# Optimization experiments

Hardware: AMD Instinct MI355X
Metric: run time of the kernel (lower is better)

## Reference

```python
import jax, jax.numpy as jnp
import numpy as np

N = 50000      # nodes
E = 800000     # edges (avg degree 16)
IN, H, OUT = 128, 128, 64


def setup_inputs() -> dict:
    key = jax.random.key(0)
    k1, k2, k3, k4 = jax.random.split(key, 4)
    x = jax.random.normal(k1, (N, IN), dtype=jnp.float32)
    edge_index = jax.random.randint(k2, (2, E), 0, N, dtype=jnp.int32)
    W1 = jax.random.normal(k3, (IN, H), dtype=jnp.float32) * (1.0 / np.sqrt(IN))
    b1 = jnp.zeros((H,), dtype=jnp.float32)
    W2 = jax.random.normal(k4, (H, OUT), dtype=jnp.float32) * (1.0 / np.sqrt(H))
    b2 = jnp.zeros((OUT,), dtype=jnp.float32)
    return {"x": x, "edge_index": edge_index, "W1": W1, "b1": b1, "W2": W2, "b2": b2}


def gcn_conv(x, edge_index, W, b):
    """PyG GCNConv: D^-1/2 (A + I) D^-1/2 (x W) + b, with self-loops."""
    src, dst = edge_index[0], edge_index[1]
    h = x @ W                                              # [N, F_out] transform first (F_out <= F_in path)
    ones = jnp.ones((src.shape[0],), dtype=h.dtype)
    deg = jax.ops.segment_sum(ones, dst, num_segments=N) + 1.0  # +1 for self-loop
    inv_sqrt_deg = jax.lax.rsqrt(deg)
    norm = inv_sqrt_deg[src] * inv_sqrt_deg[dst]           # [E]
    agg = jax.ops.segment_sum(h[src] * norm[:, None], dst, num_segments=N)
    # self-loop contribution: norm_ii = deg_i^-1
    return agg + h * (1.0 / deg)[:, None] + b


def reference(x, edge_index, W1, b1, W2, b2):
    h = jax.nn.relu(gcn_conv(x, edge_index, W1, b1))
    return gcn_conv(h, edge_index, W2, b2)
```

## Files before the change

kernel.cpp:

```cpp
#include <hip/hip_runtime.h>
#include <hip/hip_bf16.h>


#define GCN_IN   128
#define GCN_H    128
#define GCN_OUT  64
#define CAP      64
#define OVF_CAP  65536
#define SCAT_BLOCKS 2048

using short8 = __attribute__((ext_vector_type(8))) short;
using f32x4  = __attribute__((ext_vector_type(4))) float;

__device__ __forceinline__ ushort f2bf(float f) {
    uint b = __float_as_uint(f);
    b = (b + 0x7FFFu + ((b >> 16) & 1u)) >> 16;
    return (ushort)b;
}
__device__ __forceinline__ float bf2f_lo(uint u) { return __uint_as_float(u << 16); }
__device__ __forceinline__ float bf2f_hi(uint u) { return __uint_as_float(u & 0xFFFF0000u); }

__global__ __launch_bounds__(256) void k_scatter(
        const int* __restrict__ src, const int* __restrict__ dst,
        int* __restrict__ cnt, ushort* __restrict__ slot,
        int* __restrict__ ovfcnt, int2* __restrict__ ovf, int E, int N) {
    const int part = blockIdx.x & 7;
    const int psz  = (N + 7) >> 3;
    const int lo   = part * psz;
    const int hi   = min(lo + psz, N);
    const int bip  = blockIdx.x >> 3;
    const int stride = (SCAT_BLOCKS >> 3) * 256;
    for (int e = bip * 256 + threadIdx.x; e < E; e += stride) {
        int d = __builtin_nontemporal_load(dst + e);
        int s = __builtin_nontemporal_load(src + e);
        if (d >= lo && d < hi) {
            int pos = atomicAdd(&cnt[d], 1);
            if (pos < CAP) {
                slot[(size_t)d * CAP + pos] = (ushort)s;
            } else {
                int q = atomicAdd(ovfcnt, 1);
                if (q < OVF_CAP) ovf[q] = make_int2(d, s);
            }
        }
    }
}

__global__ __launch_bounds__(256) void k_gemm1(const float* __restrict__ A,
                                               const float* __restrict__ B,
                                               const int* __restrict__ cnt,
                                               ushort* __restrict__ C, int M) {
    __shared__ __align__(16) ushort As[64][136];
    __shared__ __align__(16) ushort Bs[128][136];
    const int tid  = threadIdx.x;
    const int w    = tid >> 6;
    const int lane = tid & 63;
    const int l15  = lane & 15;
    const int q8   = (lane >> 4) * 8;
    const int row0 = blockIdx.x * 64;

    #pragma unroll
    for (int t = 0; t < 8; ++t) {
        int f = tid * 4 + t * 1024;
        int r = f >> 7;
        int k = f & 127;
        float4 v = make_float4(0.f, 0.f, 0.f, 0.f);
        int gr = row0 + r;
        if (gr < M) v = *(const float4*)(A + (size_t)gr * 128 + k);
        ushort4 o;
        o.x = f2bf(v.x); o.y = f2bf(v.y); o.z = f2bf(v.z); o.w = f2bf(v.w);
        *(ushort4*)&As[r][k] = o;
    }
    #pragma unroll
    for (int t = 0; t < 16; ++t) {
        int f = tid * 4 + t * 1024;
        int k = f >> 7;
        int n = f & 127;
        float4 v = *(const float4*)(B + (size_t)k * 128 + n);
        Bs[n + 0][k] = f2bf(v.x);
        Bs[n + 1][k] = f2bf(v.y);
        Bs[n + 2][k] = f2bf(v.z);
        Bs[n + 3][k] = f2bf(v.w);
    }
    __syncthreads();

    f32x4 acc[8];
    #pragma unroll
    for (int t = 0; t < 8; ++t) {
        acc[t][0] = 0.f; acc[t][1] = 0.f; acc[t][2] = 0.f; acc[t][3] = 0.f;
    }
    #pragma unroll
    for (int kt = 0; kt < 4; ++kt) {
        short8 a = *(const short8*)&As[16 * w + l15][32 * kt + q8];
        #pragma unroll
        for (int t = 0; t < 8; ++t) {
            short8 b = *(const short8*)&Bs[16 * t + l15][32 * kt + q8];
            acc[t] = __builtin_amdgcn_mfma_f32_16x16x32_bf16(a, b, acc[t], 0, 0, 0);
        }
    }
    const int quad = lane >> 4;
    #pragma unroll
    for (int r = 0; r < 4; ++r) {
        int grow = row0 + 16 * w + quad * 4 + r;
        if (grow < M) {
            float ws = rsqrtf((float)(cnt[grow] + 1));
            #pragma unroll
            for (int t = 0; t < 8; ++t) {
                C[(size_t)grow * 128 + 16 * t + l15] = f2bf(ws * acc[t][r]);
            }
        }
    }
}

__global__ __launch_bounds__(256) void k_gemm2(const ushort* __restrict__ A,
                                               const float* __restrict__ B,
                                               const int* __restrict__ cnt,
                                               ushort* __restrict__ C, int M) {
    __shared__ __align__(16) ushort As[64][136];
    __shared__ __align__(16) ushort Bs[64][136];
    const int tid  = threadIdx.x;
    const int w    = tid >> 6;
    const int lane = tid & 63;
    const int l15  = lane & 15;
    const int q8   = (lane >> 4) * 8;
    const int row0 = blockIdx.x * 64;

    #pragma unroll
    for (int t = 0; t < 4; ++t) {
        int f = tid * 8 + t * 2048;
        int r = f >> 7;
        int k = f & 127;
        uint4 v = make_uint4(0u, 0u, 0u, 0u);
        int gr = row0 + r;
        if (gr < M) v = *(const uint4*)(A + (size_t)gr * 128 + k);
        *(uint4*)&As[r][k] = v;
    }
    #pragma unroll
    for (int t = 0; t < 8; ++t) {
        int f = tid * 4 + t * 1024;
        int k = f >> 6;
        int n = f & 63;
        float4 v = *(const float4*)(B + (size_t)k * 64 + n);
        Bs[n + 0][k] = f2bf(v.x);
        Bs[n + 1][k] = f2bf(v.y);
        Bs[n + 2][k] = f2bf(v.z);
        Bs[n + 3][k] = f2bf(v.w);
    }
    __syncthreads();

    f32x4 acc[4];
    #pragma unroll
    for (int t = 0; t < 4; ++t) {
        acc[t][0] = 0.f; acc[t][1] = 0.f; acc[t][2] = 0.f; acc[t][3] = 0.f;
    }
    #pragma unroll
    for (int kt = 0; kt < 4; ++kt) {
        short8 a = *(const short8*)&As[16 * w + l15][32 * kt + q8];
        #pragma unroll
        for (int t = 0; t < 4; ++t) {
            short8 b = *(const short8*)&Bs[16 * t + l15][32 * kt + q8];
            acc[t] = __builtin_amdgcn_mfma_f32_16x16x32_bf16(a, b, acc[t], 0, 0, 0);
        }
    }
    const int quad = lane >> 4;
    #pragma unroll
    for (int r = 0; r < 4; ++r) {
        int grow = row0 + 16 * w + quad * 4 + r;
        if (grow < M) {
            float ws = rsqrtf((float)(cnt[grow] + 1));
            #pragma unroll
            for (int t = 0; t < 4; ++t) {
                C[(size_t)grow * 64 + 16 * t + l15] = f2bf(ws * acc[t][r]);
            }
        }
    }
}

__global__ __launch_bounds__(256) void k_agg128(const ushort* __restrict__ h,
                                                const int* __restrict__ cnt,
                                                const ushort* __restrict__ slot,
                                                const float* __restrict__ bias,
                                                const int* __restrict__ ovfcnt,
                                                const int2* __restrict__ ovf,
                                                ushort* __restrict__ out, int n) {
    int node = (blockIdx.x * 256 + threadIdx.x) >> 6;
    int lane = threadIdx.x & 63;
    if (node >= n) return;
    int deg = cnt[node];
    int degm = min(deg, CAP);
    float isd_i = rsqrtf((float)(deg + 1));
    int sidx = (int)__builtin_nontemporal_load(slot + (size_t)node * CAP + lane);

    const int q = lane >> 4;
    const int i = lane & 15;
    const ushort* hp = h + 8 * i;

    float acc[8] = {};
    for (int j = 0; j < degm; j += 8) {
        int j0 = j + q;
        int j1 = j + 4 + q;
        int   s0 = __shfl(sidx, j0);
        int   s1 = __shfl(sidx, j1);
        float w0 = (j0 < degm) ? 1.f : 0.f;
        float w1 = (j1 < degm) ? 1.f : 0.f;
        uint4 v0 = *(const uint4*)(hp + (size_t)s0 * 128);
        uint4 v1 = *(const uint4*)(hp + (size_t)s1 * 128);
        acc[0] += w0 * bf2f_lo(v0.x) + w1 * bf2f_lo(v1.x);
        acc[1] += w0 * bf2f_hi(v0.x) + w1 * bf2f_hi(v1.x);
        acc[2] += w0 * bf2f_lo(v0.y) + w1 * bf2f_lo(v1.y);
        acc[3] += w0 * bf2f_hi(v0.y) + w1 * bf2f_hi(v1.y);
        acc[4] += w0 * bf2f_lo(v0.z) + w1 * bf2f_lo(v1.z);
        acc[5] += w0 * bf2f_hi(v0.z) + w1 * bf2f_hi(v1.z);
        acc[6] += w0 * bf2f_lo(v0.w) + w1 * bf2f_lo(v1.w);
        acc[7] += w0 * bf2f_hi(v0.w) + w1 * bf2f_hi(v1.w);
    }
    int ovn = *ovfcnt;
    for (int t = 0; t < ovn; ++t) {
        int2 p = ovf[t];
        if (p.x == node && q == 0) {
            uint4 v0 = *(const uint4*)(hp + (size_t)p.y * 128);
            acc[0] += bf2f_lo(v0.x); acc[1] += bf2f_hi(v0.x);
            acc[2] += bf2f_lo(v0.y); acc[3] += bf2f_hi(v0.y);
            acc[4] += bf2f_lo(v0.z); acc[5] += bf2f_hi(v0.z);
            acc[6] += bf2f_lo(v0.w); acc[7] += bf2f_hi(v0.w);
        }
    }
    #pragma unroll
    for (int k = 0; k < 8; ++k) {
        acc[k] += __shfl_xor(acc[k], 16);
        acc[k] += __shfl_xor(acc[k], 32);
    }
    if (q == 0) {
        uint4 vs = *(const uint4*)(hp + (size_t)node * 128);
        float4 ba = *(const float4*)(bias + 8 * i);
        float4 bb = *(const float4*)(bias + 8 * i + 4);
        float r0 = fmaxf((acc[0] + bf2f_lo(vs.x)) * isd_i + ba.x, 0.f);
        float r1 = fmaxf((acc[1] + bf2f_hi(vs.x)) * isd_i + ba.y, 0.f);
        float r2 = fmaxf((acc[2] + bf2f_lo(vs.y)) * isd_i + ba.z, 0.f);
        float r3 = fmaxf((acc[3] + bf2f_hi(vs.y)) * isd_i + ba.w, 0.f);
        float r4 = fmaxf((acc[4] + bf2f_lo(vs.z)) * isd_i + bb.x, 0.f);
        float r5 = fmaxf((acc[5] + bf2f_hi(vs.z)) * isd_i + bb.y, 0.f);
        float r6 = fmaxf((acc[6] + bf2f_lo(vs.w)) * isd_i + bb.z, 0.f);
        float r7 = fmaxf((acc[7] + bf2f_hi(vs.w)) * isd_i + bb.w, 0.f);
        uint4 o;
        o.x = (uint)f2bf(r0) | ((uint)f2bf(r1) << 16);
        o.y = (uint)f2bf(r2) | ((uint)f2bf(r3) << 16);
        o.z = (uint)f2bf(r4) | ((uint)f2bf(r5) << 16);
        o.w = (uint)f2bf(r6) | ((uint)f2bf(r7) << 16);
        *(uint4*)(out + (size_t)node * 128 + 8 * i) = o;
    }
}

__global__ __launch_bounds__(256) void k_agg64(const ushort* __restrict__ h,
                                               const int* __restrict__ cnt,
                                               const ushort* __restrict__ slot,
                                               const float* __restrict__ bias,
                                               const int* __restrict__ ovfcnt,
                                               const int2* __restrict__ ovf,
                                               float* __restrict__ out, int n) {
    int node = (blockIdx.x * 256 + threadIdx.x) >> 6;
    int lane = threadIdx.x & 63;
    if (node >= n) return;
    int deg = cnt[node];
    int degm = min(deg, CAP);
    float isd_i = rsqrtf((float)(deg + 1));
    int sidx = (int)__builtin_nontemporal_load(slot + (size_t)node * CAP + lane);

    const int g = lane >> 3;
    const int i = lane & 7;
    const ushort* hp = h + 8 * i;

    float acc[8] = {};
    for (int j = 0; j < degm; j += 16) {
        int j0 = j + g;
        int j1 = j + 8 + g;
        int   s0 = __shfl(sidx, j0);
        int   s1 = __shfl(sidx, j1);
        float w0 = (j0 < degm) ? 1.f : 0.f;
        float w1 = (j1 < degm) ? 1.f : 0.f;
        uint4 v0 = *(const uint4*)(hp + (size_t)s0 * 64);
        uint4 v1 = *(const uint4*)(hp + (size_t)s1 * 64);
        acc[0] += w0 * bf2f_lo(v0.x) + w1 * bf2f_lo(v1.x);
        acc[1] += w0 * bf2f_hi(v0.x) + w1 * bf2f_hi(v1.x);
        acc[2] += w0 * bf2f_lo(v0.y) + w1 * bf2f_lo(v1.y);
        acc[3] += w0 * bf2f_hi(v0.y) + w1 * bf2f_hi(v1.y);
        acc[4] += w0 * bf2f_lo(v0.z) + w1 * bf2f_lo(v1.z);
        acc[5] += w0 * bf2f_hi(v0.z) + w1 * bf2f_hi(v1.z);
        acc[6] += w0 * bf2f_lo(v0.w) + w1 * bf2f_lo(v1.w);
        acc[7] += w0 * bf2f_hi(v0.w) + w1 * bf2f_hi(v1.w);
    }
    int ovn = *ovfcnt;
    for (int t = 0; t < ovn; ++t) {
        int2 p = ovf[t];
        if (p.x == node && g == 0) {
            uint4 v0 = *(const uint4*)(hp + (size_t)p.y * 64);
            acc[0] += bf2f_lo(v0.x); acc[1] += bf2f_hi(v0.x);
            acc[2] += bf2f_lo(v0.y); acc[3] += bf2f_hi(v0.y);
            acc[4] += bf2f_lo(v0.z); acc[5] += bf2f_hi(v0.z);
            acc[6] += bf2f_lo(v0.w); acc[7] += bf2f_hi(v0.w);
        }
    }
    #pragma unroll
    for (int k = 0; k < 8; ++k) {
        acc[k] += __shfl_xor(acc[k], 8);
        acc[k] += __shfl_xor(acc[k], 16);
        acc[k] += __shfl_xor(acc[k], 32);
    }
    if (g == 0) {
        uint4 vs = *(const uint4*)(hp + (size_t)node * 64);
        float4 ba = *(const float4*)(bias + 8 * i);
        float4 bb = *(const float4*)(bias + 8 * i + 4);
        float4 r0, r1;
        r0.x = (acc[0] + bf2f_lo(vs.x)) * isd_i + ba.x;
        r0.y = (acc[1] + bf2f_hi(vs.x)) * isd_i + ba.y;
        r0.z = (acc[2] + bf2f_lo(vs.y)) * isd_i + ba.z;
        r0.w = (acc[3] + bf2f_hi(vs.y)) * isd_i + ba.w;
        r1.x = (acc[4] + bf2f_lo(vs.z)) * isd_i + bb.x;
        r1.y = (acc[5] + bf2f_hi(vs.z)) * isd_i + bb.y;
        r1.z = (acc[6] + bf2f_lo(vs.w)) * isd_i + bb.z;
        r1.w = (acc[7] + bf2f_hi(vs.w)) * isd_i + bb.w;
        float* op = out + (size_t)node * 64 + 8 * i;
        *(float4*)op = r0;
        *(float4*)(op + 4) = r1;
    }
}

static inline size_t align256(size_t x) { return (x + 255) & ~(size_t)255; }

extern "C" void kernel_launch(void* const* d_in, const int* in_sizes, int n_in,
                              void* d_out, int out_size, void* d_ws, size_t ws_size,
                              hipStream_t stream) {
    const float* x  = (const float*)d_in[0];
    const int*   ei = (const int*)d_in[1];
    const float* W1 = (const float*)d_in[2];
    const float* b1 = (const float*)d_in[3];
    const float* W2 = (const float*)d_in[4];
    const float* b2 = (const float*)d_in[5];
    float* out = (float*)d_out;

    const int N = in_sizes[0] / GCN_IN;
    const int E = in_sizes[1] / 2;
    const int* src = ei;
    const int* dst = ei + E;

    char* ws = (char*)d_ws;
    size_t o = 0;
    int*    cnt    = (int*)(ws + o);     o += align256((size_t)N * 4);
    int*    ovfcnt = (int*)(ws + o);     o += 256;
    int2*   ovf    = (int2*)(ws + o);    o += align256((size_t)OVF_CAP * 8);
    ushort* slot   = (ushort*)(ws + o);  o += align256((size_t)N * CAP * 2);
    ushort* hb     = (ushort*)(ws + o);  o += align256((size_t)N * GCN_H * 2);
    ushort* h1b    = (ushort*)(ws + o);  o += align256((size_t)N * GCN_H * 2);
    ushort* h2b    = (ushort*)(ws + o);  o += align256((size_t)N * GCN_OUT * 2);

    hipMemsetAsync(cnt, 0, align256((size_t)N * 4) + 256, stream);

    k_scatter<<<SCAT_BLOCKS, 256, 0, stream>>>(src, dst, cnt, slot,
                                               ovfcnt, ovf, E, N);

    k_gemm1<<<(N + 63) / 64, 256, 0, stream>>>(x, W1, cnt, hb, N);

    k_agg128<<<(N * 64 + 255) / 256, 256, 0, stream>>>(hb, cnt, slot, b1,
                                                       ovfcnt, ovf, h1b, N);
    k_gemm2<<<(N + 63) / 64, 256, 0, stream>>>(h1b, W2, cnt, h2b, N);

    k_agg64<<<(N * 64 + 255) / 256, 256, 0, stream>>>(h2b, cnt, slot, b2,
                                                      ovfcnt, ovf, out, N);
}
```

Measured before the change: 205.6 us.

## Bucket neighbor slots by source range and compact overflow into slots

The scatter now reads four edges at a time with vector loads and splits each node's 64 slots into 8 buckets of 8, chosen by source-id range. The goal is rough source ordering inside each adjacency row and less contention on a single per-node counter. A new compaction kernel packs the buckets with ballot/popcount, merges overflow edges into the slot row, and writes the final degree and clamped degree. Both aggregation kernels drop their per-node linear scan of the overflow list. The cost is an extra kernel launch and an 8x larger counter array to clear and read. The vector loads also assume E is a multiple of 4.

```diff
diff --git a/kernel.cpp b/kernel.cpp
--- a/kernel.cpp
+++ b/kernel.cpp
@@ -5,12 +5,12 @@
 #define GCN_IN   128
 #define GCN_H    128
 #define GCN_OUT  64
-#define CAP      64
 #define OVF_CAP  65536
 #define SCAT_BLOCKS 2048
 
 using short8 = __attribute__((ext_vector_type(8))) short;
 using f32x4  = __attribute__((ext_vector_type(4))) float;
+using int4v  = __attribute__((ext_vector_type(4))) int;
 
 __device__ __forceinline__ ushort f2bf(float f) {
     uint b = __float_as_uint(f);
@@ -22,26 +22,71 @@
 
 __global__ __launch_bounds__(256) void k_scatter(
         const int* __restrict__ src, const int* __restrict__ dst,
-        int* __restrict__ cnt, ushort* __restrict__ slot,
-        int* __restrict__ ovfcnt, int2* __restrict__ ovf, int E, int N) {
+        int* __restrict__ cnt8, ushort* __restrict__ slot,
+        int* __restrict__ ovfcnt, int2* __restrict__ ovf,
+        int E, int N, float pscale) {
     const int part = blockIdx.x & 7;
     const int psz  = (N + 7) >> 3;
     const int lo   = part * psz;
     const int hi   = min(lo + psz, N);
     const int bip  = blockIdx.x >> 3;
-    const int stride = (SCAT_BLOCKS >> 3) * 256;
-    for (int e = bip * 256 + threadIdx.x; e < E; e += stride) {
-        int d = __builtin_nontemporal_load(dst + e);
-        int s = __builtin_nontemporal_load(src + e);
-        if (d >= lo && d < hi) {
-            int pos = atomicAdd(&cnt[d], 1);
-            if (pos < CAP) {
-                slot[(size_t)d * CAP + pos] = (ushort)s;
-            } else {
-                int q = atomicAdd(ovfcnt, 1);
-                if (q < OVF_CAP) ovf[q] = make_int2(d, s);
+    const int stride4 = (SCAT_BLOCKS >> 3) * 256 * 4;
+    for (int e = (bip * 256 + threadIdx.x) * 4; e < E; e += stride4) {
+        int4v d4 = __builtin_nontemporal_load((const int4v*)(dst + e));
+        int4v s4 = __builtin_nontemporal_load((const int4v*)(src + e));
+        #pragma unroll
+        for (int k = 0; k < 4; ++k) {
+            int d = d4[k];
+            int s = s4[k];
+            if (d >= lo && d < hi) {
+                int p = min((int)((float)s * pscale), 7);
+                int pos = atomicAdd(&cnt8[d * 8 + p], 1);
+                if (pos < 8) {
+                    slot[(size_t)d * 64 + p * 8 + pos] = (ushort)s;
+                } else {
+                    int q = atomicAdd(ovfcnt, 1);
+                    if (q < OVF_CAP) ovf[q] = make_int2(d, s);
+                }
             }
         }
+    }
+}
+
+__global__ __launch_bounds__(256) void k_compact(
+        ushort* __restrict__ slot, const int* __restrict__ cnt8,
+        int* __restrict__ cnt, int* __restrict__ degs,
+        const int* __restrict__ ovfcnt, const int2* __restrict__ ovf, int N) {
+    int node = (blockIdx.x * 256 + threadIdx.x) >> 6;
+    int lane = threadIdx.x & 63;
+    if (node >= N) return;
+    int np = cnt8[node * 8 + (lane >> 3)];
+    bool valid = (lane & 7) < np;
+    ushort v = slot[(size_t)node * 64 + lane];
+    unsigned long long mask = __ballot(valid);
+    int total = __popcll(mask);
+    int pos = __popcll(mask & ((1ull << lane) - 1ull));
+    if (valid) slot[(size_t)node * 64 + pos] = v;
+    int appended = 0;
+    int ovn = *ovfcnt;
+    for (int q = 0; q < ovn; q += 64) {
+        int ex = -1, ey = 0;
+        if (q + lane < ovn) {
+            int2 e = ovf[q + lane];
+            ex = e.x; ey = e.y;
+        }
+        bool m = (ex == node);
+        unsigned long long mb = __ballot(m);
+        if (m) {
+            int ai = __popcll(mb & ((1ull << lane) - 1ull));
+            int wp = total + appended + ai;
+            if (wp < 64) slot[(size_t)node * 64 + wp] = (ushort)ey;
+        }
+        appended += __popcll(mb);
+    }
+    if (lane == 0) {
+        int deg = total + appended;
+        cnt[node]  = deg;
+        degs[node] = min(deg, 64);
     }
 }
 
@@ -177,18 +222,16 @@
 
 __global__ __launch_bounds__(256) void k_agg128(const ushort* __restrict__ h,
                                                 const int* __restrict__ cnt,
+                                                const int* __restrict__ degs,
                                                 const ushort* __restrict__ slot,
                                                 const float* __restrict__ bias,
-                                                const int* __restrict__ ovfcnt,
-                                                const int2* __restrict__ ovf,
                                                 ushort* __restrict__ out, int n) {
     int node = (blockIdx.x * 256 + threadIdx.x) >> 6;
     int lane = threadIdx.x & 63;
     if (node >= n) return;
-    int deg = cnt[node];
-    int degm = min(deg, CAP);
-    float isd_i = rsqrtf((float)(deg + 1));
-    int sidx = (int)__builtin_nontemporal_load(slot + (size_t)node * CAP + lane);
+    int degm = degs[node];
+    float isd_i = rsqrtf((float)(cnt[node] + 1));
+    int sidx = (int)__builtin_nontemporal_load(slot + (size_t)node * 64 + lane);
 
     const int q = lane >> 4;
     const int i = lane & 15;
@@ -213,17 +256,6 @@
         acc[6] += w0 * bf2f_lo(v0.w) + w1 * bf2f_lo(v1.w);
         acc[7] += w0 * bf2f_hi(v0.w) + w1 * bf2f_hi(v1.w);
     }
-    int ovn = *ovfcnt;
-    for (int t = 0; t < ovn; ++t) {
-        int2 p = ovf[t];
-        if (p.x == node && q == 0) {
-            uint4 v0 = *(const uint4*)(hp + (size_t)p.y * 128);
-            acc[0] += bf2f_lo(v0.x); acc[1] += bf2f_hi(v0.x);
-            acc[2] += bf2f_lo(v0.y); acc[3] += bf2f_hi(v0.y);
-            acc[4] += bf2f_lo(v0.z); acc[5] += bf2f_hi(v0.z);
-            acc[6] += bf2f_lo(v0.w); acc[7] += bf2f_hi(v0.w);
-        }
-    }
     #pragma unroll
     for (int k = 0; k < 8; ++k) {
         acc[k] += __shfl_xor(acc[k], 16);
@@ -252,18 +284,16 @@
 
 __global__ __launch_bounds__(256) void k_agg64(const ushort* __restrict__ h,
                                                const int* __restrict__ cnt,
+                                               const int* __restrict__ degs,
                                                const ushort* __restrict__ slot,
                                                const float* __restrict__ bias,
-                                               const int* __restrict__ ovfcnt,
-                                               const int2* __restrict__ ovf,
                                                float* __restrict__ out, int n) {
     int node = (blockIdx.x * 256 + threadIdx.x) >> 6;
     int lane = threadIdx.x & 63;
     if (node >= n) return;
-    int deg = cnt[node];
-    int degm = min(deg, CAP);
-    float isd_i = rsqrtf((float)(deg + 1));
-    int sidx = (int)__builtin_nontemporal_load(slot + (size_t)node * CAP + lane);
+    int degm = degs[node];
+    float isd_i = rsqrtf((float)(cnt[node] + 1));
+    int sidx = (int)__builtin_nontemporal_load(slot + (size_t)node * 64 + lane);
 
     const int g = lane >> 3;
     const int i = lane & 7;
@@ -288,17 +318,6 @@
         acc[6] += w0 * bf2f_lo(v0.w) + w1 * bf2f_lo(v1.w);
         acc[7] += w0 * bf2f_hi(v0.w) + w1 * bf2f_hi(v1.w);
     }
-    int ovn = *ovfcnt;
-    for (int t = 0; t < ovn; ++t) {
-        int2 p = ovf[t];
-        if (p.x == node && g == 0) {
-            uint4 v0 = *(const uint4*)(hp + (size_t)p.y * 64);
-            acc[0] += bf2f_lo(v0.x); acc[1] += bf2f_hi(v0.x);
-            acc[2] += bf2f_lo(v0.y); acc[3] += bf2f_hi(v0.y);
-            acc[4] += bf2f_lo(v0.z); acc[5] += bf2f_hi(v0.z);
-            acc[6] += bf2f_lo(v0.w); acc[7] += bf2f_hi(v0.w);
-        }
-    }
     #pragma unroll
     for (int k = 0; k < 8; ++k) {
         acc[k] += __shfl_xor(acc[k], 8);
@@ -344,25 +363,30 @@
 
     char* ws = (char*)d_ws;
     size_t o = 0;
-    int*    cnt    = (int*)(ws + o);     o += align256((size_t)N * 4);
+    int*    cnt8   = (int*)(ws + o);     o += align256((size_t)N * 8 * 4);
     int*    ovfcnt = (int*)(ws + o);     o += 256;
     int2*   ovf    = (int2*)(ws + o);    o += align256((size_t)OVF_CAP * 8);
-    ushort* slot   = (ushort*)(ws + o);  o += align256((size_t)N * CAP * 2);
+    ushort* slot   = (ushort*)(ws + o);  o += align256((size_t)N * 64 * 2);
+    int*    cnt    = (int*)(ws + o);     o += align256((size_t)N * 4);
+    int*    degs   = (int*)(ws + o);     o += align256((size_t)N * 4);
     ushort* hb     = (ushort*)(ws + o);  o += align256((size_t)N * GCN_H * 2);
     ushort* h1b    = (ushort*)(ws + o);  o += align256((size_t)N * GCN_H * 2);
     ushort* h2b    = (ushort*)(ws + o);  o += align256((size_t)N * GCN_OUT * 2);
 
-    hipMemsetAsync(cnt, 0, align256((size_t)N * 4) + 256, stream);
-
-    k_scatter<<<SCAT_BLOCKS, 256, 0, stream>>>(src, dst, cnt, slot,
-                                               ovfcnt, ovf, E, N);
+    (void)hipMemsetAsync(cnt8, 0, align256((size_t)N * 8 * 4) + 256, stream);
+
+    k_scatter<<<SCAT_BLOCKS, 256, 0, stream>>>(src, dst, cnt8, slot,
+                                               ovfcnt, ovf, E, N, 8.0f / (float)N);
+
+    k_compact<<<(N * 64 + 255) / 256, 256, 0, stream>>>(slot, cnt8, cnt, degs,
+                                                        ovfcnt, ovf, N);
 
     k_gemm1<<<(N + 63) / 64, 256, 0, stream>>>(x, W1, cnt, hb, N);
 
-    k_agg128<<<(N * 64 + 255) / 256, 256, 0, stream>>>(hb, cnt, slot, b1,
-                                                       ovfcnt, ovf, h1b, N);
+    k_agg128<<<(N * 64 + 255) / 256, 256, 0, stream>>>(hb, cnt, degs, slot, b1,
+                                                       h1b, N);
     k_gemm2<<<(N + 63) / 64, 256, 0, stream>>>(h1b, W2, cnt, h2b, N);
 
-    k_agg64<<<(N * 64 + 255) / 256, 256, 0, stream>>>(h2b, cnt, slot, b2,
-                                                      ovfcnt, ovf, out, N);
-}
+    k_agg64<<<(N * 64 + 255) / 256, 256, 0, stream>>>(h2b, cnt, degs, slot, b2,
+                                                      out, N);
+}
```

Result: slower. 216.2 us (+5.1%).

## Fuse scatter with GEMM1 and fold GEMM2 into layer-1 aggregation

Applied to the files above, without the earlier changes.

Merges the edge scatter and the first GEMM into one launch so they run side by side. Because the GEMM no longer waits for degrees, source-side normalization moves into the aggregation as per-neighbor weights gathered from cnt. The second GEMM is folded into the layer-1 aggregation kernel: each wave's aggregated row goes to LDS and is multiplied by W2 with scalar FMAs. This drops one launch and the h1 round trip through memory, at the cost of extra per-edge cnt gathers, a W2 reload into LDS per 4-node block, and scalar dot products in place of MFMA.

```diff
diff --git a/kernel.cpp b/kernel.cpp
--- a/kernel.cpp
+++ b/kernel.cpp
@@ -11,6 +11,7 @@
 
 using short8 = __attribute__((ext_vector_type(8))) short;
 using f32x4  = __attribute__((ext_vector_type(4))) float;
+using int4v  = __attribute__((ext_vector_type(4))) int;
 
 __device__ __forceinline__ ushort f2bf(float f) {
     uint b = __float_as_uint(f);
@@ -20,233 +21,217 @@
 __device__ __forceinline__ float bf2f_lo(uint u) { return __uint_as_float(u << 16); }
 __device__ __forceinline__ float bf2f_hi(uint u) { return __uint_as_float(u & 0xFFFF0000u); }
 
-__global__ __launch_bounds__(256) void k_scatter(
+__global__ __launch_bounds__(256) void k_fused1(
         const int* __restrict__ src, const int* __restrict__ dst,
         int* __restrict__ cnt, ushort* __restrict__ slot,
-        int* __restrict__ ovfcnt, int2* __restrict__ ovf, int E, int N) {
-    const int part = blockIdx.x & 7;
-    const int psz  = (N + 7) >> 3;
-    const int lo   = part * psz;
-    const int hi   = min(lo + psz, N);
-    const int bip  = blockIdx.x >> 3;
-    const int stride = (SCAT_BLOCKS >> 3) * 256;
-    for (int e = bip * 256 + threadIdx.x; e < E; e += stride) {
-        int d = __builtin_nontemporal_load(dst + e);
-        int s = __builtin_nontemporal_load(src + e);
-        if (d >= lo && d < hi) {
-            int pos = atomicAdd(&cnt[d], 1);
-            if (pos < CAP) {
-                slot[(size_t)d * CAP + pos] = (ushort)s;
-            } else {
-                int q = atomicAdd(ovfcnt, 1);
-                if (q < OVF_CAP) ovf[q] = make_int2(d, s);
+        int* __restrict__ ovfcnt, int2* __restrict__ ovf, int E,
+        const float* __restrict__ A, const float* __restrict__ B,
+        ushort* __restrict__ C, int M, int N) {
+    __shared__ __align__(16) ushort As[64][40];
+    __shared__ __align__(16) ushort Bs[128][40];
+    const int tid = threadIdx.x;
+
+    if (blockIdx.x < SCAT_BLOCKS) {
+        const int part = blockIdx.x & 7;
+        const int psz  = (N + 7) >> 3;
+        const int lo   = part * psz;
+        const int hi   = min(lo + psz, N);
+        const int bip  = blockIdx.x >> 3;
+        const int stride4 = (SCAT_BLOCKS >> 3) * 256 * 4;
+        for (int e = (bip * 256 + tid) * 4; e < E; e += stride4) {
+            int4v d4 = __builtin_nontemporal_load((const int4v*)(dst + e));
+            int4v s4 = __builtin_nontemporal_load((const int4v*)(src + e));
+            #pragma unroll
+            for (int k = 0; k < 4; ++k) {
+                int d = d4[k];
+                int s = s4[k];
+                if (d >= lo && d < hi) {
+                    int pos = atomicAdd(&cnt[d], 1);
+                    if (pos < CAP) {
+                        slot[(size_t)d * CAP + pos] = (ushort)s;
+                    } else {
+                        int q = atomicAdd(ovfcnt, 1);
+                        if (q < OVF_CAP) ovf[q] = make_int2(d, s);
+                    }
+                }
             }
         }
-    }
-}
-
-__global__ __launch_bounds__(256) void k_gemm1(const float* __restrict__ A,
-                                               const float* __restrict__ B,
-                                               const int* __restrict__ cnt,
-                                               ushort* __restrict__ C, int M) {
-    __shared__ __align__(16) ushort As[64][136];
-    __shared__ __align__(16) ushort Bs[128][136];
-    const int tid  = threadIdx.x;
+        return;
+    }
+
+    const int g    = blockIdx.x - SCAT_BLOCKS;
+    const int row0 = g * 64;
     const int w    = tid >> 6;
     const int lane = tid & 63;
     const int l15  = lane & 15;
     const int q8   = (lane >> 4) * 8;
-    const int row0 = blockIdx.x * 64;
-
-    #pragma unroll
-    for (int t = 0; t < 8; ++t) {
-        int f = tid * 4 + t * 1024;
-        int r = f >> 7;
-        int k = f & 127;
-        float4 v = make_float4(0.f, 0.f, 0.f, 0.f);
-        int gr = row0 + r;
-        if (gr < M) v = *(const float4*)(A + (size_t)gr * 128 + k);
-        ushort4 o;
-        o.x = f2bf(v.x); o.y = f2bf(v.y); o.z = f2bf(v.z); o.w = f2bf(v.w);
-        *(ushort4*)&As[r][k] = o;
-    }
-    #pragma unroll
-    for (int t = 0; t < 16; ++t) {
-        int f = tid * 4 + t * 1024;
-        int k = f >> 7;
-        int n = f & 127;
-        float4 v = *(const float4*)(B + (size_t)k * 128 + n);
-        Bs[n + 0][k] = f2bf(v.x);
-        Bs[n + 1][k] = f2bf(v.y);
-        Bs[n + 2][k] = f2bf(v.z);
-        Bs[n + 3][k] = f2bf(v.w);
-    }
-    __syncthreads();
 
     f32x4 acc[8];
     #pragma unroll
     for (int t = 0; t < 8; ++t) {
         acc[t][0] = 0.f; acc[t][1] = 0.f; acc[t][2] = 0.f; acc[t][3] = 0.f;
     }
-    #pragma unroll
-    for (int kt = 0; kt < 4; ++kt) {
-        short8 a = *(const short8*)&As[16 * w + l15][32 * kt + q8];
+    for (int kb = 0; kb < 128; kb += 32) {
+        #pragma unroll
+        for (int tt = 0; tt < 2; ++tt) {
+            int f = tid * 4 + tt * 1024;
+            int r = f >> 5;
+            int k = f & 31;
+            float4 v = make_float4(0.f, 0.f, 0.f, 0.f);
+            int gr = row0 + r;
+            if (gr < M) v = *(const float4*)(A + (size_t)gr * 128 + kb + k);
+            ushort4 o;
+            o.x = f2bf(v.x); o.y = f2bf(v.y); o.z = f2bf(v.z); o.w = f2bf(v.w);
+            *(ushort4*)&As[r][k] = o;
+        }
+        #pragma unroll
+        for (int tt = 0; tt < 4; ++tt) {
+            int f = tid * 4 + tt * 1024;
+            int k = f >> 7;
+            int n = f & 127;
+            float4 v = *(const float4*)(B + (size_t)(kb + k) * 128 + n);
+            Bs[n + 0][k] = f2bf(v.x);
+            Bs[n + 1][k] = f2bf(v.y);
+            Bs[n + 2][k] = f2bf(v.z);
+            Bs[n + 3][k] = f2bf(v.w);
+        }
+        __syncthreads();
+        short8 a = *(const short8*)&As[16 * w + l15][q8];
         #pragma unroll
         for (int t = 0; t < 8; ++t) {
-            short8 b = *(const short8*)&Bs[16 * t + l15][32 * kt + q8];
+            short8 b = *(const short8*)&Bs[16 * t + l15][q8];
             acc[t] = __builtin_amdgcn_mfma_f32_16x16x32_bf16(a, b, acc[t], 0, 0, 0);
         }
+        __syncthreads();
     }
     const int quad = lane >> 4;
     #pragma unroll
     for (int r = 0; r < 4; ++r) {
         int grow = row0 + 16 * w + quad * 4 + r;
         if (grow < M) {
-            float ws = rsqrtf((float)(cnt[grow] + 1));
             #pragma unroll
             for (int t = 0; t < 8; ++t) {
-                C[(size_t)grow * 128 + 16 * t + l15] = f2bf(ws * acc[t][r]);
+                __builtin_nontemporal_store(
+                    f2bf(acc[t][r]), C + (size_t)grow * 128 + 16 * t + l15);
             }
         }
     }
 }
 
-__global__ __launch_bounds__(256) void k_gemm2(const ushort* __restrict__ A,
-                                               const float* __restrict__ B,
-                                               const int* __restrict__ cnt,
-                                               ushort* __restrict__ C, int M) {
-    __shared__ __align__(16) ushort As[64][136];
-    __shared__ __align__(16) ushort Bs[64][136];
+__global__ __launch_bounds__(256) void k_agg128g2(
+        const ushort* __restrict__ h,
+        const int* __restrict__ cnt,
+        const ushort* __restrict__ slot,
+        const float* __restrict__ bias,
+        const int* __restrict__ ovfcnt,
+        const int2* __restrict__ ovf,
+        const float* __restrict__ W2,
+        ushort* __restrict__ h2b,
+        int n) {
+    __shared__ __align__(16) ushort W2s[64][136];
+    __shared__ __align__(16) ushort h1s[4][136];
     const int tid  = threadIdx.x;
     const int w    = tid >> 6;
     const int lane = tid & 63;
-    const int l15  = lane & 15;
-    const int q8   = (lane >> 4) * 8;
-    const int row0 = blockIdx.x * 64;
+    const int node = blockIdx.x * 4 + w;
 
     #pragma unroll
-    for (int t = 0; t < 4; ++t) {
-        int f = tid * 8 + t * 2048;
-        int r = f >> 7;
-        int k = f & 127;
-        uint4 v = make_uint4(0u, 0u, 0u, 0u);
-        int gr = row0 + r;
-        if (gr < M) v = *(const uint4*)(A + (size_t)gr * 128 + k);
-        *(uint4*)&As[r][k] = v;
-    }
-    #pragma unroll
-    for (int t = 0; t < 8; ++t) {
-        int f = tid * 4 + t * 1024;
+    for (int tt = 0; tt < 8; ++tt) {
+        int f = tid * 4 + tt * 1024;
         int k = f >> 6;
-        int n = f & 63;
-        float4 v = *(const float4*)(B + (size_t)k * 64 + n);
-        Bs[n + 0][k] = f2bf(v.x);
-        Bs[n + 1][k] = f2bf(v.y);
-        Bs[n + 2][k] = f2bf(v.z);
-        Bs[n + 3][k] = f2bf(v.w);
+        int nn = f & 63;
+        float4 v = *(const float4*)(W2 + (size_t)k * 64 + nn);
+        W2s[nn + 0][k] = f2bf(v.x);
+        W2s[nn + 1][k] = f2bf(v.y);
+        W2s[nn + 2][k] = f2bf(v.z);
+        W2s[nn + 3][k] = f2bf(v.w);
+    }
+
+    float isd_i = 0.f;
+    if (node < n) {
+        int deg = cnt[node];
+        int degm = min(deg, CAP);
+        isd_i = rsqrtf((float)(deg + 1));
+        int sidx = (int)__builtin_nontemporal_load(slot + (size_t)node * CAP + lane);
+        bool valid = lane < degm;
+        if (!valid) sidx = 0;
+        float wl = valid ? rsqrtf((float)(cnt[sidx] + 1)) : 0.f;
+
+        const int q = lane >> 4;
+        const int i = lane & 15;
+        const ushort* hp = h + 8 * i;
+
+        float acc[8] = {};
+        for (int j = 0; j < degm; j += 8) {
+            int j0 = j + q;
+            int j1 = j + 4 + q;
+            int   s0 = __shfl(sidx, j0);
+            int   s1 = __shfl(sidx, j1);
+            float w0 = __shfl(wl, j0);
+            float w1 = __shfl(wl, j1);
+            uint4 v0 = *(const uint4*)(hp + (size_t)s0 * 128);
+            uint4 v1 = *(const uint4*)(hp + (size_t)s1 * 128);
+            acc[0] += w0 * bf2f_lo(v0.x) + w1 * bf2f_lo(v1.x);
+            acc[1] += w0 * bf2f_hi(v0.x) + w1 * bf2f_hi(v1.x);
+            acc[2] += w0 * bf2f_lo(v0.y) + w1 * bf2f_lo(v1.y);
+            acc[3] += w0 * bf2f_hi(v0.y) + w1 * bf2f_hi(v1.y);
+            acc[4] += w0 * bf2f_lo(v0.z) + w1 * bf2f_lo(v1.z);
+            acc[5] += w0 * bf2f_hi(v0.z) + w1 * bf2f_hi(v1.z);
+            acc[6] += w0 * bf2f_lo(v0.w) + w1 * bf2f_lo(v1.w);
+            acc[7] += w0 * bf2f_hi(v0.w) + w1 * bf2f_hi(v1.w);
+        }
+        int ovn = *ovfcnt;
+        for (int t = 0; t < ovn; ++t) {
+            int2 p = ovf[t];
+            if (p.x == node && q == 0) {
+                float w0 = rsqrtf((float)(cnt[p.y] + 1));
+                uint4 v0 = *(const uint4*)(hp + (size_t)p.y * 128);
+                acc[0] += w0 * bf2f_lo(v0.x); acc[1] += w0 * bf2f_hi(v0.x);
+                acc[2] += w0 * bf2f_lo(v0.y); acc[3] += w0 * bf2f_hi(v0.y);
+                acc[4] += w0 * bf2f_lo(v0.z); acc[5] += w0 * bf2f_hi(v0.z);
+                acc[6] += w0 * bf2f_lo(v0.w); acc[7] += w0 * bf2f_hi(v0.w);
+            }
+        }
+        #pragma unroll
+        for (int k = 0; k < 8; ++k) {
+            acc[k] += __shfl_xor(acc[k], 16);
+            acc[k] += __shfl_xor(acc[k], 32);
+        }
+        if (q == 0) {
+            uint4 vs = *(const uint4*)(hp + (size_t)node * 128);
+            float4 ba = *(const float4*)(bias + 8 * i);
+            float4 bb = *(const float4*)(bias + 8 * i + 4);
+            float r0 = fmaxf((acc[0] + isd_i * bf2f_lo(vs.x)) * isd_i + ba.x, 0.f);
+            float r1 = fmaxf((acc[1] + isd_i * bf2f_hi(vs.x)) * isd_i + ba.y, 0.f);
+            float r2 = fmaxf((acc[2] + isd_i * bf2f_lo(vs.y)) * isd_i + ba.z, 0.f);
+            float r3 = fmaxf((acc[3] + isd_i * bf2f_hi(vs.y)) * isd_i + ba.w, 0.f);
+            float r4 = fmaxf((acc[4] + isd_i * bf2f_lo(vs.z)) * isd_i + bb.x, 0.f);
+            float r5 = fmaxf((acc[5] + isd_i * bf2f_hi(vs.z)) * isd_i + bb.y, 0.f);
+            float r6 = fmaxf((acc[6] + isd_i * bf2f_lo(vs.w)) * isd_i + bb.z, 0.f);
+            float r7 = fmaxf((acc[7] + isd_i * bf2f_hi(vs.w)) * isd_i + bb.w, 0.f);
+            uint4 o;
+            o.x = (uint)f2bf(r0) | ((uint)f2bf(r1) << 16);
+            o.y = (uint)f2bf(r2) | ((uint)f2bf(r3) << 16);
+            o.z = (uint)f2bf(r4) | ((uint)f2bf(r5) << 16);
+            o.w = (uint)f2bf(r6) | ((uint)f2bf(r7) << 16);
+            *(uint4*)&h1s[w][8 * i] = o;
+        }
     }
     __syncthreads();
 
-    f32x4 acc[4];
-    #pragma unroll
-    for (int t = 0; t < 4; ++t) {
-        acc[t][0] = 0.f; acc[t][1] = 0.f; acc[t][2] = 0.f; acc[t][3] = 0.f;
-    }
-    #pragma unroll
-    for (int kt = 0; kt < 4; ++kt) {
-        short8 a = *(const short8*)&As[16 * w + l15][32 * kt + q8];
-        #pragma unroll
-        for (int t = 0; t < 4; ++t) {
-            short8 b = *(const short8*)&Bs[16 * t + l15][32 * kt + q8];
-            acc[t] = __builtin_amdgcn_mfma_f32_16x16x32_bf16(a, b, acc[t], 0, 0, 0);
-        }
-    }
-    const int quad = lane >> 4;
-    #pragma unroll
-    for (int r = 0; r < 4; ++r) {
-        int grow = row0 + 16 * w + quad * 4 + r;
-        if (grow < M) {
-            float ws = rsqrtf((float)(cnt[grow] + 1));
-            #pragma unroll
-            for (int t = 0; t < 4; ++t) {
-                C[(size_t)grow * 64 + 16 * t + l15] = f2bf(ws * acc[t][r]);
-            }
-        }
-    }
-}
-
-__global__ __launch_bounds__(256) void k_agg128(const ushort* __restrict__ h,
-                                                const int* __restrict__ cnt,
-                                                const ushort* __restrict__ slot,
-                                                const float* __restrict__ bias,
-                                                const int* __restrict__ ovfcnt,
-                                                const int2* __restrict__ ovf,
-                                                ushort* __restrict__ out, int n) {
-    int node = (blockIdx.x * 256 + threadIdx.x) >> 6;
-    int lane = threadIdx.x & 63;
-    if (node >= n) return;
-    int deg = cnt[node];
-    int degm = min(deg, CAP);
-    float isd_i = rsqrtf((float)(deg + 1));
-    int sidx = (int)__builtin_nontemporal_load(slot + (size_t)node * CAP + lane);
-
-    const int q = lane >> 4;
-    const int i = lane & 15;
-    const ushort* hp = h + 8 * i;
-
-    float acc[8] = {};
-    for (int j = 0; j < degm; j += 8) {
-        int j0 = j + q;
-        int j1 = j + 4 + q;
-        int   s0 = __shfl(sidx, j0);
-        int   s1 = __shfl(sidx, j1);
-        float w0 = (j0 < degm) ? 1.f : 0.f;
-        float w1 = (j1 < degm) ? 1.f : 0.f;
-        uint4 v0 = *(const uint4*)(hp + (size_t)s0 * 128);
-        uint4 v1 = *(const uint4*)(hp + (size_t)s1 * 128);
-        acc[0] += w0 * bf2f_lo(v0.x) + w1 * bf2f_lo(v1.x);
-        acc[1] += w0 * bf2f_hi(v0.x) + w1 * bf2f_hi(v1.x);
-        acc[2] += w0 * bf2f_lo(v0.y) + w1 * bf2f_lo(v1.y);
-        acc[3] += w0 * bf2f_hi(v0.y) + w1 * bf2f_hi(v1.y);
-        acc[4] += w0 * bf2f_lo(v0.z) + w1 * bf2f_lo(v1.z);
-        acc[5] += w0 * bf2f_hi(v0.z) + w1 * bf2f_hi(v1.z);
-        acc[6] += w0 * bf2f_lo(v0.w) + w1 * bf2f_lo(v1.w);
-        acc[7] += w0 * bf2f_hi(v0.w) + w1 * bf2f_hi(v1.w);
-    }
-    int ovn = *ovfcnt;
-    for (int t = 0; t < ovn; ++t) {
-        int2 p = ovf[t];
-        if (p.x == node && q == 0) {
-            uint4 v0 = *(const uint4*)(hp + (size_t)p.y * 128);
-            acc[0] += bf2f_lo(v0.x); acc[1] += bf2f_hi(v0.x);
-            acc[2] += bf2f_lo(v0.y); acc[3] += bf2f_hi(v0.y);
-            acc[4] += bf2f_lo(v0.z); acc[5] += bf2f_hi(v0.z);
-            acc[6] += bf2f_lo(v0.w); acc[7] += bf2f_hi(v0.w);
-        }
-    }
-    #pragma unroll
-    for (int k = 0; k < 8; ++k) {
-        acc[k] += __shfl_xor(acc[k], 16);
-        acc[k] += __shfl_xor(acc[k], 32);
-    }
-    if (q == 0) {
-        uint4 vs = *(const uint4*)(hp + (size_t)node * 128);
-        float4 ba = *(const float4*)(bias + 8 * i);
-        float4 bb = *(const float4*)(bias + 8 * i + 4);
-        float r0 = fmaxf((acc[0] + bf2f_lo(vs.x)) * isd_i + ba.x, 0.f);
-        float r1 = fmaxf((acc[1] + bf2f_hi(vs.x)) * isd_i + ba.y, 0.f);
-        float r2 = fmaxf((acc[2] + bf2f_lo(vs.y)) * isd_i + ba.z, 0.f);
-        float r3 = fmaxf((acc[3] + bf2f_hi(vs.y)) * isd_i + ba.w, 0.f);
-        float r4 = fmaxf((acc[4] + bf2f_lo(vs.z)) * isd_i + bb.x, 0.f);
-        float r5 = fmaxf((acc[5] + bf2f_hi(vs.z)) * isd_i + bb.y, 0.f);
-        float r6 = fmaxf((acc[6] + bf2f_lo(vs.w)) * isd_i + bb.z, 0.f);
-        float r7 = fmaxf((acc[7] + bf2f_hi(vs.w)) * isd_i + bb.w, 0.f);
-        uint4 o;
-        o.x = (uint)f2bf(r0) | ((uint)f2bf(r1) << 16);
-        o.y = (uint)f2bf(r2) | ((uint)f2bf(r3) << 16);
-        o.z = (uint)f2bf(r4) | ((uint)f2bf(r5) << 16);
-        o.w = (uint)f2bf(r6) | ((uint)f2bf(r7) << 16);
-        *(uint4*)(out + (size_t)node * 128 + 8 * i) = o;
+    if (node < n) {
+        float s = 0.f;
+        #pragma unroll
+        for (int kk = 0; kk < 16; ++kk) {
+            uint4 hv = *(const uint4*)&h1s[w][8 * kk];
+            uint4 wv = *(const uint4*)&W2s[lane][8 * kk];
+            s += bf2f_lo(hv.x) * bf2f_lo(wv.x) + bf2f_hi(hv.x) * bf2f_hi(wv.x);
+            s += bf2f_lo(hv.y) * bf2f_lo(wv.y) + bf2f_hi(hv.y) * bf2f_hi(wv.y);
+            s += bf2f_lo(hv.z) * bf2f_lo(wv.z) + bf2f_hi(hv.z) * bf2f_hi(wv.z);
+            s += bf2f_lo(hv.w) * bf2f_lo(wv.w) + bf2f_hi(hv.w) * bf2f_hi(wv.w);
+        }
+        __builtin_nontemporal_store(f2bf(isd_i * s),
+                                    h2b + (size_t)node * 64 + lane);
     }
 }
 
@@ -349,19 +334,18 @@
     int2*   ovf    = (int2*)(ws + o);    o += align256((size_t)OVF_CAP * 8);
     ushort* slot   = (ushort*)(ws + o);  o += align256((size_t)N * CAP * 2);
     ushort* hb     = (ushort*)(ws + o);  o += align256((size_t)N * GCN_H * 2);
-    ushort* h1b    = (ushort*)(ws + o);  o += align256((size_t)N * GCN_H * 2);
     ushort* h2b    = (ushort*)(ws + o);  o += align256((size_t)N * GCN_OUT * 2);
 
-    hipMemsetAsync(cnt, 0, align256((size_t)N * 4) + 256, stream);
-
-    k_scatter<<<SCAT_BLOCKS, 256, 0, stream>>>(src, dst, cnt, slot,
-                                               ovfcnt, ovf, E, N);
-
-    k_gemm1<<<(N + 63) / 64, 256, 0, stream>>>(x, W1, cnt, hb, N);
-
-    k_agg128<<<(N * 64 + 255) / 256, 256, 0, stream>>>(hb, cnt, slot, b1,
-                                                       ovfcnt, ovf, h1b, N);
-    k_gemm2<<<(N + 63) / 64, 256, 0, stream>>>(h1b, W2, cnt, h2b, N);
+    (void)hipMemsetAsync(cnt, 0, align256((size_t)N * 4) + 256, stream);
+
+    {
+        int gemm_blocks = (N + 63) / 64;
+        k_fused1<<<SCAT_BLOCKS + gemm_blocks, 256, 0, stream>>>(
+            src, dst, cnt, slot, ovfcnt, ovf, E, x, W1, hb, N, N);
+    }
+
+    k_agg128g2<<<(N + 3) / 4, 256, 0, stream>>>(hb, cnt, slot, b1,
+                                                ovfcnt, ovf, W2, h2b, N);
 
     k_agg64<<<(N * 64 + 255) / 256, 256, 0, stream>>>(h2b, cnt, slot, b2,
                                                       ovfcnt, ovf, out, N);
```

Result: slower. 232.7 us (+13.2%).
